# Kernel optimization log

Hardware: AMD Instinct MI355X
Metric: run time of the kernel (lower is better)

The kernel has to match this reference:

```python
import jax, jax.numpy as jnp
import numpy as np

H = 32
W = 32
N = H * W            # num_patches = 1024
DIM = 512
HEADS = 8
DH = 64              # dim_head
INNER = HEADS * DH
B = 4
GATE = -2.0          # fixed, requires_grad=False in the torch module
NEG_THRESH = 0.9


def _rel_pos_index_dis():
    # mirrors relative_pos_index_dis(height=32, weight=32)
    coords = np.stack(np.meshgrid(np.arange(H), np.arange(W), indexing='ij'))  # [2,H,W]
    flat = coords.reshape(2, -1)                      # [2, N]
    rel = flat[:, :, None] - flat[:, None, :]         # [2, N, N]
    rel = rel.transpose(1, 2, 0).copy()               # [N, N, 2]
    dis = (rel[..., 0].astype(np.float32) / H) ** 2 + (rel[..., 1].astype(np.float32) / W) ** 2
    rel[..., 0] += H - 1
    rel[..., 1] += W - 1
    rel[..., 0] *= 2 * W - 1
    idx = rel.sum(-1)
    return idx.astype(np.int32), dis.astype(np.float32)


def setup_inputs() -> dict:
    key = jax.random.key(0)
    ks = jax.random.split(key, 6)
    rpi, dis = _rel_pos_index_dis()
    return {
        'x': jax.random.normal(ks[0], (B, N, DIM), dtype=jnp.float32),
        'prob': jax.random.uniform(ks[1], (B, N), dtype=jnp.float32),
        'w_qkv': jax.random.normal(ks[2], (DIM, 3 * INNER), dtype=jnp.float32) * 0.02,
        'rpb_table': jax.random.normal(ks[3], ((2 * H - 1) * (2 * W - 1), HEADS), dtype=jnp.float32) * 0.02,
        'headsita': jnp.arange(1, HEADS + 1, dtype=jnp.float32) * 0.1,
        'w_thresh': jax.random.normal(ks[4], (DH,), dtype=jnp.float32) * 0.02,
        'w_out': jax.random.normal(ks[5], (INNER, DIM), dtype=jnp.float32) * 0.02,
        'b_out': jnp.zeros((DIM,), dtype=jnp.float32),
        'rpi': jnp.asarray(rpi),
        'dis': jnp.asarray(dis),
    }


def reference(x, prob, w_qkv, rpb_table, headsita, w_thresh, w_out, b_out, rpi, dis):
    b, n, _ = x.shape
    h = headsita.shape[0]
    d = w_thresh.shape[0]
    scale = d ** -0.5

    qkv = x @ w_qkv                                            # [b, n, 3*h*d]
    q, k, v = jnp.split(qkv, 3, axis=-1)
    to_heads = lambda t: t.reshape(b, n, h, d).transpose(0, 2, 1, 3)  # [b, h, n, d]
    q, k, v = to_heads(q), to_heads(k), to_heads(v)

    dots0 = jnp.einsum('bhid,bhjd->bhij', q, k) * scale        # [b, h, n, n]

    # RPE: table lookup bias + learned Gaussian distance bias
    rpb = rpb_table[rpi.reshape(-1)].reshape(n, n, h).transpose(2, 0, 1)  # [h, n, n]
    factor = 1.0 / (2.0 * headsita ** 2 + 1e-6)                # [h]
    pos = jnp.exp(-factor[:, None, None] * dis[None, :, :])    # [h, n, n]
    dots = dots0 + rpb[None] + 0.01 * pos[None]

    attn = jax.nn.softmax(dots, axis=-1)                       # [b, h, n, n]
    attn_max = attn.max(axis=-1)                               # [b, h, n]
    attn_min = attn.min(axis=-1)

    # per-query learned threshold, gated by sigmoid(gate)
    t = jax.nn.sigmoid(jnp.einsum('bhnd,d->bhn', q, w_thresh)) * jax.nn.sigmoid(GATE)
    thresh = attn_min + t * (attn_max - attn_min)               # [b, h, n]

    record = (attn - thresh[..., None] > 0).astype(attn.dtype)  # hard 0/1 mask
    # rows (queries) whose prob >= neg_thresh are fully zeroed (as in the torch code)
    record = record * (prob < NEG_THRESH)[:, None, :, None].astype(attn.dtype)

    deno = jnp.sum(attn * record, axis=-1)                      # [b, h, n]
    attn_p = attn * record / (deno[..., None] + 1e-6)

    out = jnp.einsum('bhij,bhjd->bhid', attn_p, v)              # [b, h, n, d]
    out = out.transpose(0, 2, 1, 3).reshape(b, n, h * d)
    out = out @ w_out + b_out                                   # [b, n, dim]
    return out, jax.nn.softmax(dots0, axis=-1)
```

## Files before the change

kernel.cpp:

```cpp
#include <hip/hip_runtime.h>


__device__ __forceinline__ float wsum(float v) {
#pragma unroll
  for (int off = 32; off > 0; off >>= 1) v += __shfl_xor(v, off, 64);
  return v;
}
__device__ __forceinline__ float wmaxr(float v) {
#pragma unroll
  for (int off = 32; off > 0; off >>= 1) v = fmaxf(v, __shfl_xor(v, off, 64));
  return v;
}
__device__ __forceinline__ float wminr(float v) {
#pragma unroll
  for (int off = 32; off > 0; off >>= 1) v = fminf(v, __shfl_xor(v, off, 64));
  return v;
}

__global__ void build_btab(const float* __restrict__ rpb,
                           const float* __restrict__ headsita,
                           float* __restrict__ btab) {
  const int h = blockIdx.y;
  const int flat = blockIdx.x * 256 + threadIdx.x;
  if (flat >= 3969) return;
  const float sita = headsita[h];
  const float factor = 1.0f / (2.0f * sita * sita + 1e-6f);
  const int dy = flat / 63 - 31;
  const int dx = flat % 63 - 31;
  const float fy = (float)dy * 0.03125f, fx = (float)dx * 0.03125f;
  btab[h * 3969 + flat] =
      rpb[(size_t)flat * 8 + h] + 0.01f * __expf(-factor * (fy * fy + fx * fx));
}

__global__ __launch_bounds__(256) void gemm_f32_128(
    const float* __restrict__ A, const float* __restrict__ Bm,
    float* __restrict__ C, int M, int N, int K) {
  __shared__ float As[16][132];
  __shared__ float Bs[16][132];
  const int t = threadIdx.x;
  const int bm = blockIdx.y * 128;
  const int bn = blockIdx.x * 128;
  const int tx = t & 15;
  const int ty = t >> 4;

  float acc[8][8];
#pragma unroll
  for (int i = 0; i < 8; ++i)
#pragma unroll
    for (int j = 0; j < 8; ++j) acc[i][j] = 0.0f;

  const int mr = t >> 1;
  const int kc = (t & 1) * 8;
  const int kr = t >> 4;
  const int nc = (t & 15) * 8;

  for (int k0 = 0; k0 < K; k0 += 16) {
    const float4* asrc = (const float4*)&A[(size_t)(bm + mr) * K + k0 + kc];
    const float4 a0 = asrc[0], a1 = asrc[1];
    const float4* bsrc = (const float4*)&Bm[(size_t)(k0 + kr) * N + bn + nc];
    const float4 b0 = bsrc[0], b1 = bsrc[1];
    __syncthreads();
    As[kc + 0][mr] = a0.x; As[kc + 1][mr] = a0.y;
    As[kc + 2][mr] = a0.z; As[kc + 3][mr] = a0.w;
    As[kc + 4][mr] = a1.x; As[kc + 5][mr] = a1.y;
    As[kc + 6][mr] = a1.z; As[kc + 7][mr] = a1.w;
    *(float4*)&Bs[kr][nc] = b0;
    *(float4*)&Bs[kr][nc + 4] = b1;
    __syncthreads();
#pragma unroll
    for (int kk = 0; kk < 16; ++kk) {
      const float4 aLo = *(const float4*)&As[kk][ty * 4];
      const float4 aHi = *(const float4*)&As[kk][64 + ty * 4];
      const float4 bLo = *(const float4*)&Bs[kk][tx * 4];
      const float4 bHi = *(const float4*)&Bs[kk][64 + tx * 4];
      const float av[8] = {aLo.x, aLo.y, aLo.z, aLo.w, aHi.x, aHi.y, aHi.z, aHi.w};
      const float bv[8] = {bLo.x, bLo.y, bLo.z, bLo.w, bHi.x, bHi.y, bHi.z, bHi.w};
#pragma unroll
      for (int i = 0; i < 8; ++i)
#pragma unroll
        for (int j = 0; j < 8; ++j) acc[i][j] += av[i] * bv[j];
    }
  }

#pragma unroll
  for (int i = 0; i < 8; ++i) {
    const int row = bm + ((i < 4) ? (ty * 4 + i) : (64 + ty * 4 + (i - 4)));
    float4 lo, hi;
    lo.x = acc[i][0]; lo.y = acc[i][1]; lo.z = acc[i][2]; lo.w = acc[i][3];
    hi.x = acc[i][4]; hi.y = acc[i][5]; hi.z = acc[i][6]; hi.w = acc[i][7];
    *(float4*)&C[(size_t)row * N + bn + tx * 4] = lo;
    *(float4*)&C[(size_t)row * N + bn + 64 + tx * 4] = hi;
  }
}

__global__ __launch_bounds__(256, 3) void attn_fused(
    const float* __restrict__ qkv,
    const float* __restrict__ prob,
    const float* __restrict__ btab,
    const float* __restrict__ w_thresh,
    float* __restrict__ out2,
    float* __restrict__ attnout)
{
  __shared__ float kv_lds[128 * 64];
  __shared__ float q_t[64 * 36];
  __shared__ float multi[2048];

  const int t = threadIdx.x;
  const int w = t >> 6, l = t & 63;
  const int id = blockIdx.y * 32 + blockIdx.x;
  const int work = (id & 7) * 128 + (id >> 3);
  const int bh = work >> 5;
  const int itile = work & 31;
  const int b = bh >> 3, h = bh & 7;
  const int i0 = itile * 32;
  const int yi = itile;

  const float* bsl = btab + h * 3969 + yi * 63;
#pragma unroll
  for (int c = 0; c < 8; ++c) {
    const int e = c * 256 + t;
    if (e < 2016) multi[e] = bsl[e];
  }
#pragma unroll
  for (int c = 0; c < 8; ++c) {
    const int idx = c * 256 + t;
    const int row = idx >> 6, d = idx & 63;
    q_t[d * 36 + row] = qkv[(size_t)(b * 1024 + i0 + row) * 1536 + h * 64 + d];
  }
  __syncthreads();

  const float wt = w_thresh[l];
  float tval[8];
#pragma unroll
  for (int r = 0; r < 8; ++r) {
    const int row = w * 8 + r;
    const float v = wsum(q_t[l * 36 + row] * wt);
    float tv = (1.0f / (1.0f + __expf(-v))) * 0.11920292202211755f;
    tv += (prob[b * 1024 + i0 + row] >= 0.9f) ? 2.0f : 0.0f;
    tval[r] = tv;
  }

  float s[8][16];
#pragma unroll
  for (int r = 0; r < 8; ++r)
#pragma unroll
    for (int tt = 0; tt < 16; ++tt) s[r][tt] = 0.0f;

  const size_t kbase = (size_t)b * 1024 * 1536 + 512 + h * 64;
  const int swl = l & 31;
#pragma unroll
  for (int jt = 0; jt < 8; ++jt) {
    __syncthreads();
#pragma unroll
    for (int c = 0; c < 8; ++c) {
      const int f = (c * 256 + t) * 4;
      const int j = f >> 6, dd = f & 63;
      const float4 v4 = *(const float4*)&qkv[kbase + (size_t)(jt * 128 + j) * 1536 + dd];
      const int sw = j & 31;
      kv_lds[j * 64 + ((dd + 0) ^ sw)] = v4.x;
      kv_lds[j * 64 + ((dd + 1) ^ sw)] = v4.y;
      kv_lds[j * 64 + ((dd + 2) ^ sw)] = v4.z;
      kv_lds[j * 64 + ((dd + 3) ^ sw)] = v4.w;
    }
    __syncthreads();
#pragma unroll 8
    for (int d = 0; d < 64; ++d) {
      const float kv0 = kv_lds[l * 64 + (d ^ swl)];
      const float kv1 = kv_lds[(64 + l) * 64 + (d ^ swl)];
      const float4 qA = *(const float4*)&q_t[d * 36 + w * 8];
      const float4 qB = *(const float4*)&q_t[d * 36 + w * 8 + 4];
      const float qa[8] = {qA.x, qA.y, qA.z, qA.w, qB.x, qB.y, qB.z, qB.w};
#pragma unroll
      for (int r = 0; r < 8; ++r) {
        s[r][jt * 2 + 0] += qa[r] * kv0;
        s[r][jt * 2 + 1] += qa[r] * kv1;
      }
    }
  }

  const size_t o2base = ((size_t)(b * 8 + h)) << 20;
#pragma unroll
  for (int r = 0; r < 8; ++r) {
#pragma unroll
    for (int tt = 0; tt < 16; ++tt) s[r][tt] *= 0.125f;
    float m = -1e30f;
#pragma unroll
    for (int tt = 0; tt < 16; ++tt) m = fmaxf(m, s[r][tt]);
    m = wmaxr(m);
    float e[16];
    float sum = 0.0f;
#pragma unroll
    for (int tt = 0; tt < 16; ++tt) { e[tt] = __expf(s[r][tt] - m); sum += e[tt]; }
    sum = wsum(sum);
    const float inv = 1.0f / sum;
    float* orow = out2 + o2base + (size_t)(i0 + w * 8 + r) * 1024;
#pragma unroll
    for (int tt = 0; tt < 16; ++tt)
      __builtin_nontemporal_store(e[tt] * inv, &orow[tt * 64 + l]);
  }

#pragma unroll
  for (int r = 0; r < 8; ++r) {
    const int xi = (w * 8 + r) & 31;
#pragma unroll
    for (int tt = 0; tt < 16; ++tt) {
      const int j = tt * 64 + l;
      const int yj = j >> 5, xj = j & 31;
      s[r][tt] += multi[(31 - yj) * 63 + (xi - xj + 31)];
    }
  }

#pragma unroll
  for (int r = 0; r < 8; ++r) {
    float m = -1e30f, mn = 1e30f;
#pragma unroll
    for (int tt = 0; tt < 16; ++tt) { m = fmaxf(m, s[r][tt]); mn = fminf(mn, s[r][tt]); }
    m = wmaxr(m); mn = wminr(mn);
    float sum = 0.0f;
#pragma unroll
    for (int tt = 0; tt < 16; ++tt) { const float e = __expf(s[r][tt] - m); s[r][tt] = e; sum += e; }
    sum = wsum(sum);
    const float emin = __expf(mn - m);
    const float th_e = emin + tval[r] * (1.0f - emin);
    float deno = 0.0f;
#pragma unroll
    for (int tt = 0; tt < 16; ++tt) {
      const float a = (s[r][tt] > th_e) ? s[r][tt] : 0.0f;
      s[r][tt] = a;
      deno += a;
    }
    deno = wsum(deno);
    const float invden = 1.0f / (deno + 1e-6f * sum);
#pragma unroll
    for (int tt = 0; tt < 16; ++tt) s[r][tt] *= invden;
  }

  float outv[8];
#pragma unroll
  for (int r = 0; r < 8; ++r) outv[r] = 0.0f;
  const size_t vbase = (size_t)b * 1024 * 1536 + 1024 + h * 64;
#pragma unroll
  for (int jt = 0; jt < 8; ++jt) {
    __syncthreads();
#pragma unroll
    for (int c = 0; c < 8; ++c) {
      const int f = (c * 256 + t) * 4;
      const int j = f >> 6, dd = f & 63;
      const float4 v4 = *(const float4*)&qkv[vbase + (size_t)(jt * 128 + j) * 1536 + dd];
      const int sw = j & 31;
      kv_lds[j * 64 + ((dd + 0) ^ sw)] = v4.x;
      kv_lds[j * 64 + ((dd + 1) ^ sw)] = v4.y;
      kv_lds[j * 64 + ((dd + 2) ^ sw)] = v4.z;
      kv_lds[j * 64 + ((dd + 3) ^ sw)] = v4.w;
    }
    __syncthreads();
#pragma unroll
    for (int h2 = 0; h2 < 2; ++h2) {
#pragma unroll
      for (int r = 0; r < 8; ++r) multi[w * 512 + r * 64 + l] = s[r][jt * 2 + h2];
#pragma unroll 4
      for (int j0 = 0; j0 < 64; j0 += 4) {
        const int jb = h2 * 64 + j0;
        const float v0 = kv_lds[(jb + 0) * 64 + (l ^ ((jb + 0) & 31))];
        const float v1 = kv_lds[(jb + 1) * 64 + (l ^ ((jb + 1) & 31))];
        const float v2 = kv_lds[(jb + 2) * 64 + (l ^ ((jb + 2) & 31))];
        const float v3 = kv_lds[(jb + 3) * 64 + (l ^ ((jb + 3) & 31))];
#pragma unroll
        for (int r = 0; r < 8; ++r) {
          const float4 p4 = *(const float4*)&multi[w * 512 + r * 64 + j0];
          outv[r] += p4.x * v0 + p4.y * v1 + p4.z * v2 + p4.w * v3;
        }
      }
    }
  }
#pragma unroll
  for (int r = 0; r < 8; ++r)
    attnout[(size_t)(b * 1024 + i0 + w * 8 + r) * 512 + h * 64 + l] = outv[r];
}

__global__ __launch_bounds__(256) void gemm_f32_64_bias(
    const float* __restrict__ A, const float* __restrict__ Bm,
    const float* __restrict__ bias, float* __restrict__ C,
    int M, int N, int K) {
  __shared__ float As[16][68];
  __shared__ float Bs[16][68];
  const int t = threadIdx.x;
  const int bm = blockIdx.y * 64;
  const int bn = blockIdx.x * 64;
  const int tx = t & 15;
  const int ty = t >> 4;

  float acc[4][4];
#pragma unroll
  for (int i = 0; i < 4; ++i)
#pragma unroll
    for (int j = 0; j < 4; ++j) acc[i][j] = 0.0f;

  const int amr = t >> 2;
  const int akc = (t & 3) * 4;
  const int bkr = t >> 4;
  const int bnc = (t & 15) * 4;

  for (int k0 = 0; k0 < K; k0 += 16) {
    const float4 a0 = *(const float4*)&A[(size_t)(bm + amr) * K + k0 + akc];
    const float4 b0 = *(const float4*)&Bm[(size_t)(k0 + bkr) * N + bn + bnc];
    __syncthreads();
    As[akc + 0][amr] = a0.x; As[akc + 1][amr] = a0.y;
    As[akc + 2][amr] = a0.z; As[akc + 3][amr] = a0.w;
    *(float4*)&Bs[bkr][bnc] = b0;
    __syncthreads();
#pragma unroll
    for (int kk = 0; kk < 16; ++kk) {
      const float4 av = *(const float4*)&As[kk][ty * 4];
      const float4 bv = *(const float4*)&Bs[kk][tx * 4];
      const float aa[4] = {av.x, av.y, av.z, av.w};
      const float bb[4] = {bv.x, bv.y, bv.z, bv.w};
#pragma unroll
      for (int i = 0; i < 4; ++i)
#pragma unroll
        for (int j = 0; j < 4; ++j) acc[i][j] += aa[i] * bb[j];
    }
  }

  const float4 bi = *(const float4*)&bias[bn + tx * 4];
#pragma unroll
  for (int i = 0; i < 4; ++i) {
    float4 o;
    o.x = acc[i][0] + bi.x; o.y = acc[i][1] + bi.y;
    o.z = acc[i][2] + bi.z; o.w = acc[i][3] + bi.w;
    *(float4*)&C[(size_t)(bm + ty * 4 + i) * N + bn + tx * 4] = o;
  }
}

extern "C" void kernel_launch(void* const* d_in, const int* in_sizes, int n_in,
                              void* d_out, int out_size, void* d_ws, size_t ws_size,
                              hipStream_t stream) {
  const float* x        = (const float*)d_in[0];
  const float* prob     = (const float*)d_in[1];
  const float* w_qkv    = (const float*)d_in[2];
  const float* rpb      = (const float*)d_in[3];
  const float* headsita = (const float*)d_in[4];
  const float* w_thresh = (const float*)d_in[5];
  const float* w_out    = (const float*)d_in[6];
  const float* b_out    = (const float*)d_in[7];

  float* out  = (float*)d_out;
  float* out2 = out + (size_t)4 * 1024 * 512;

  float* qkv     = (float*)d_ws;
  float* attnout = qkv + (size_t)4 * 1024 * 1536;
  float* btab    = attnout + (size_t)4 * 1024 * 512;

  build_btab<<<dim3(16, 8), 256, 0, stream>>>(rpb, headsita, btab);

  gemm_f32_128<<<dim3(1536 / 128, 4096 / 128), 256, 0, stream>>>(
      x, w_qkv, qkv, 4096, 1536, 512);

  attn_fused<<<dim3(32, 32), 256, 0, stream>>>(
      qkv, prob, btab, w_thresh, out2, attnout);

  gemm_f32_64_bias<<<dim3(512 / 64, 4096 / 64), 256, 0, stream>>>(
      attnout, w_out, b_out, out, 4096, 512, 512);
}
```

Measured before the change: 634.6 us.

## Restructure attention LDS layouts with float4 K reads and readlane-based PV accumulation

The QK^T loop now stages K as 256 rows by 32 dims per pass with an XOR-swizzled float4 layout. Q is stored row-major with padding, so both operands are read as float4 vectors. The PV stage drops the shared-memory round trip for probabilities. Each lane's score is broadcast with readlane, and V tiles are loaded unswizzled, 64 rows at a time. The intent is fewer LDS instructions and bank conflicts. The costs are more barriers in the V loop, 64 serial readlanes per tile, an extra exp recomputation in the first softmax, and occupancy lowered from 3 to 2 waves.

Result: no change. 634.9 us (+0.0%).

```diff
diff --git a/kernel.cpp b/kernel.cpp
--- a/kernel.cpp
+++ b/kernel.cpp
@@ -93,7 +93,7 @@
   }
 }
 
-__global__ __launch_bounds__(256, 3) void attn_fused(
+__global__ __launch_bounds__(256, 2) void attn_fused(
     const float* __restrict__ qkv,
     const float* __restrict__ prob,
     const float* __restrict__ btab,
@@ -101,9 +101,9 @@
     float* __restrict__ out2,
     float* __restrict__ attnout)
 {
-  __shared__ float kv_lds[128 * 64];
-  __shared__ float q_t[64 * 36];
-  __shared__ float multi[2048];
+  __shared__ float kv[8192];
+  __shared__ float qrow[32 * 72];
+  __shared__ float bt[2016];
 
   const int t = threadIdx.x;
   const int w = t >> 6, l = t & 63;
@@ -113,19 +113,18 @@
   const int itile = work & 31;
   const int b = bh >> 3, h = bh & 7;
   const int i0 = itile * 32;
-  const int yi = itile;
-
-  const float* bsl = btab + h * 3969 + yi * 63;
+
+  const float* bsl = btab + h * 3969 + itile * 63;
 #pragma unroll
   for (int c = 0; c < 8; ++c) {
     const int e = c * 256 + t;
-    if (e < 2016) multi[e] = bsl[e];
+    if (e < 2016) bt[e] = bsl[e];
   }
 #pragma unroll
   for (int c = 0; c < 8; ++c) {
     const int idx = c * 256 + t;
     const int row = idx >> 6, d = idx & 63;
-    q_t[d * 36 + row] = qkv[(size_t)(b * 1024 + i0 + row) * 1536 + h * 64 + d];
+    qrow[row * 72 + d] = qkv[(size_t)(b * 1024 + i0 + row) * 1536 + h * 64 + d];
   }
   __syncthreads();
 
@@ -134,7 +133,7 @@
 #pragma unroll
   for (int r = 0; r < 8; ++r) {
     const int row = w * 8 + r;
-    const float v = wsum(q_t[l * 36 + row] * wt);
+    const float v = wsum(qrow[row * 72 + l] * wt);
     float tv = (1.0f / (1.0f + __expf(-v))) * 0.11920292202211755f;
     tv += (prob[b * 1024 + i0 + row] >= 0.9f) ? 2.0f : 0.0f;
     tval[r] = tv;
@@ -147,33 +146,34 @@
     for (int tt = 0; tt < 16; ++tt) s[r][tt] = 0.0f;
 
   const size_t kbase = (size_t)b * 1024 * 1536 + 512 + h * 64;
-  const int swl = l & 31;
-#pragma unroll
-  for (int jt = 0; jt < 8; ++jt) {
-    __syncthreads();
-#pragma unroll
-    for (int c = 0; c < 8; ++c) {
-      const int f = (c * 256 + t) * 4;
-      const int j = f >> 6, dd = f & 63;
-      const float4 v4 = *(const float4*)&qkv[kbase + (size_t)(jt * 128 + j) * 1536 + dd];
-      const int sw = j & 31;
-      kv_lds[j * 64 + ((dd + 0) ^ sw)] = v4.x;
-      kv_lds[j * 64 + ((dd + 1) ^ sw)] = v4.y;
-      kv_lds[j * 64 + ((dd + 2) ^ sw)] = v4.z;
-      kv_lds[j * 64 + ((dd + 3) ^ sw)] = v4.w;
-    }
-    __syncthreads();
-#pragma unroll 8
-    for (int d = 0; d < 64; ++d) {
-      const float kv0 = kv_lds[l * 64 + (d ^ swl)];
-      const float kv1 = kv_lds[(64 + l) * 64 + (d ^ swl)];
-      const float4 qA = *(const float4*)&q_t[d * 36 + w * 8];
-      const float4 qB = *(const float4*)&q_t[d * 36 + w * 8 + 4];
-      const float qa[8] = {qA.x, qA.y, qA.z, qA.w, qB.x, qB.y, qB.z, qB.w};
-#pragma unroll
-      for (int r = 0; r < 8; ++r) {
-        s[r][jt * 2 + 0] += qa[r] * kv0;
-        s[r][jt * 2 + 1] += qa[r] * kv1;
+  const int l7 = l & 7;
+#pragma unroll
+  for (int jt = 0; jt < 4; ++jt) {
+    for (int dh = 0; dh < 2; ++dh) {
+      __syncthreads();
+#pragma unroll
+      for (int c = 0; c < 8; ++c) {
+        const int q = c * 256 + t;
+        const int j = q >> 3;
+        const int dd = (q & 7) * 4;
+        const float4 va = *(const float4*)&qkv[kbase + (size_t)(jt * 256 + j) * 1536 + dh * 32 + dd];
+        *(float4*)&kv[j * 32 + 4 * ((dd >> 2) ^ (j & 7))] = va;
+      }
+      __syncthreads();
+      for (int d0 = 0; d0 < 32; d0 += 4) {
+        const int g = 4 * ((d0 >> 2) ^ l7);
+        const float4 k0 = *(const float4*)&kv[l * 32 + g];
+        const float4 k1 = *(const float4*)&kv[(64 + l) * 32 + g];
+        const float4 k2 = *(const float4*)&kv[(128 + l) * 32 + g];
+        const float4 k3 = *(const float4*)&kv[(192 + l) * 32 + g];
+#pragma unroll
+        for (int r = 0; r < 8; ++r) {
+          const float4 q4 = *(const float4*)&qrow[(w * 8 + r) * 72 + dh * 32 + d0];
+          s[r][jt * 4 + 0] = fmaf(q4.w, k0.w, fmaf(q4.z, k0.z, fmaf(q4.y, k0.y, fmaf(q4.x, k0.x, s[r][jt * 4 + 0]))));
+          s[r][jt * 4 + 1] = fmaf(q4.w, k1.w, fmaf(q4.z, k1.z, fmaf(q4.y, k1.y, fmaf(q4.x, k1.x, s[r][jt * 4 + 1]))));
+          s[r][jt * 4 + 2] = fmaf(q4.w, k2.w, fmaf(q4.z, k2.z, fmaf(q4.y, k2.y, fmaf(q4.x, k2.x, s[r][jt * 4 + 2]))));
+          s[r][jt * 4 + 3] = fmaf(q4.w, k3.w, fmaf(q4.z, k3.z, fmaf(q4.y, k3.y, fmaf(q4.x, k3.x, s[r][jt * 4 + 3]))));
+        }
       }
     }
   }
@@ -187,26 +187,25 @@
 #pragma unroll
     for (int tt = 0; tt < 16; ++tt) m = fmaxf(m, s[r][tt]);
     m = wmaxr(m);
-    float e[16];
     float sum = 0.0f;
 #pragma unroll
-    for (int tt = 0; tt < 16; ++tt) { e[tt] = __expf(s[r][tt] - m); sum += e[tt]; }
+    for (int tt = 0; tt < 16; ++tt) sum += __expf(s[r][tt] - m);
     sum = wsum(sum);
     const float inv = 1.0f / sum;
     float* orow = out2 + o2base + (size_t)(i0 + w * 8 + r) * 1024;
 #pragma unroll
     for (int tt = 0; tt < 16; ++tt)
-      __builtin_nontemporal_store(e[tt] * inv, &orow[tt * 64 + l]);
+      __builtin_nontemporal_store(__expf(s[r][tt] - m) * inv, &orow[tt * 64 + l]);
   }
 
 #pragma unroll
   for (int r = 0; r < 8; ++r) {
-    const int xi = (w * 8 + r) & 31;
+    const int xi = w * 8 + r;
 #pragma unroll
     for (int tt = 0; tt < 16; ++tt) {
       const int j = tt * 64 + l;
       const int yj = j >> 5, xj = j & 31;
-      s[r][tt] += multi[(31 - yj) * 63 + (xi - xj + 31)];
+      s[r][tt] += bt[(31 - yj) * 63 + (xi - xj + 31)];
     }
   }
 
@@ -240,36 +239,24 @@
   for (int r = 0; r < 8; ++r) outv[r] = 0.0f;
   const size_t vbase = (size_t)b * 1024 * 1536 + 1024 + h * 64;
 #pragma unroll
-  for (int jt = 0; jt < 8; ++jt) {
-    __syncthreads();
-#pragma unroll
-    for (int c = 0; c < 8; ++c) {
+  for (int tt = 0; tt < 16; ++tt) {
+    __syncthreads();
+#pragma unroll
+    for (int c = 0; c < 4; ++c) {
       const int f = (c * 256 + t) * 4;
       const int j = f >> 6, dd = f & 63;
-      const float4 v4 = *(const float4*)&qkv[vbase + (size_t)(jt * 128 + j) * 1536 + dd];
-      const int sw = j & 31;
-      kv_lds[j * 64 + ((dd + 0) ^ sw)] = v4.x;
-      kv_lds[j * 64 + ((dd + 1) ^ sw)] = v4.y;
-      kv_lds[j * 64 + ((dd + 2) ^ sw)] = v4.z;
-      kv_lds[j * 64 + ((dd + 3) ^ sw)] = v4.w;
-    }
-    __syncthreads();
-#pragma unroll
-    for (int h2 = 0; h2 < 2; ++h2) {
-#pragma unroll
-      for (int r = 0; r < 8; ++r) multi[w * 512 + r * 64 + l] = s[r][jt * 2 + h2];
+      *(float4*)&kv[j * 64 + dd] =
+          *(const float4*)&qkv[vbase + (size_t)(tt * 64 + j) * 1536 + dd];
+    }
+    __syncthreads();
 #pragma unroll 4
-      for (int j0 = 0; j0 < 64; j0 += 4) {
-        const int jb = h2 * 64 + j0;
-        const float v0 = kv_lds[(jb + 0) * 64 + (l ^ ((jb + 0) & 31))];
-        const float v1 = kv_lds[(jb + 1) * 64 + (l ^ ((jb + 1) & 31))];
-        const float v2 = kv_lds[(jb + 2) * 64 + (l ^ ((jb + 2) & 31))];
-        const float v3 = kv_lds[(jb + 3) * 64 + (l ^ ((jb + 3) & 31))];
-#pragma unroll
-        for (int r = 0; r < 8; ++r) {
-          const float4 p4 = *(const float4*)&multi[w * 512 + r * 64 + j0];
-          outv[r] += p4.x * v0 + p4.y * v1 + p4.z * v2 + p4.w * v3;
-        }
+    for (int jl = 0; jl < 64; ++jl) {
+      const float vv = kv[jl * 64 + l];
+#pragma unroll
+      for (int r = 0; r < 8; ++r) {
+        const float pv = __int_as_float(
+            __builtin_amdgcn_readlane(__float_as_int(s[r][tt]), jl));
+        outv[r] = fmaf(pv, vv, outv[r]);
       }
     }
   }
```
